# Performance work log

Measured on AMD Instinct MI355X. Metric: run time of the kernel, lower is better.

The kernel has to match this reference:

```python
import jax, jax.numpy as jnp
import numpy as np

N_NODES = 500_000
N_EDGES = 16_000_000


def setup_inputs() -> dict:
    key = jax.random.key(0)
    ks = jax.random.split(key, 10)
    x = jax.random.normal(ks[0], (N_NODES, 8), dtype=jnp.float32)
    edge_index = jax.random.randint(ks[1], (2, N_EDGES), 0, N_NODES, dtype=jnp.int64)
    W1_l = jax.random.normal(ks[2], (8, 32), dtype=jnp.float32) * 0.1
    W1_r = jax.random.normal(ks[3], (8, 32), dtype=jnp.float32) * 0.1
    b1 = jax.random.normal(ks[4], (32,), dtype=jnp.float32) * 0.1
    W2_l = jax.random.normal(ks[5], (32, 16), dtype=jnp.float32) * 0.1
    W2_r = jax.random.normal(ks[6], (32, 16), dtype=jnp.float32) * 0.1
    b2 = jax.random.normal(ks[7], (16,), dtype=jnp.float32) * 0.1
    W_out = jax.random.normal(ks[8], (16, 1), dtype=jnp.float32) * 0.1
    b_out = jax.random.normal(ks[9], (1,), dtype=jnp.float32) * 0.1
    return {"x": x, "edge_index": edge_index, "W1_l": W1_l, "W1_r": W1_r, "b1": b1,
            "W2_l": W2_l, "W2_r": W2_r, "b2": b2, "W_out": W_out, "b_out": b_out}


def _sage_conv(x, src, dst, deg_inv, W_l, W_r, b):
    # mean-aggregate neighbor features: gather x[src], scatter-add to dst, divide by degree
    agg = jax.ops.segment_sum(x[src], dst, num_segments=N_NODES)  # [N, d_in]
    mean_nb = agg * deg_inv[:, None]
    return mean_nb @ W_l + x @ W_r + b


def reference(x, edge_index, W1_l, W1_r, b1, W2_l, W2_r, b2, W_out, b_out):
    src, dst = edge_index[0], edge_index[1]
    # in-degree per target node (mean aggregation denominator), clamped at 1
    deg = jax.ops.segment_sum(jnp.ones((src.shape[0],), dtype=x.dtype), dst,
                              num_segments=N_NODES)
    deg_inv = 1.0 / jnp.maximum(deg, 1.0)
    h = jax.nn.relu(_sage_conv(x, src, dst, deg_inv, W1_l, W1_r, b1))
    # dropout(p=0.1) is identity at inference
    h = jax.nn.relu(_sage_conv(h, src, dst, deg_inv, W2_l, W2_r, b2))
    return jax.nn.sigmoid(h @ W_out + b_out)  # [N, 1]
```

## Files before the change

kernel.cpp:

```cpp
#include <hip/hip_runtime.h>
#include <hip/hip_fp16.h>
#include <math.h>

#define N_NODES 500000
#define N_EDGES 16000000

#define NCHUNK 256
#define CHUNK_E 62500
#define NBUCKET 2048
#define NPB 256
#define NB_USED 1954
#define BUCKET_CAP 9216

#define OFF_GH    0
#define OFF_TOT   2097152
#define OFF_BASE  2105344
#define OFF_ROW   2113600
#define OFF_DEG   4113600
#define OFF_XH8   6113600
#define OFF_PAIRS 10113664
#define OFF_H1P8  74113664
#define OFF_S2    82113664

typedef float v2f __attribute__((ext_vector_type(2)));

static __device__ inline float2 up2(unsigned int u) {
  __half2 h = *reinterpret_cast<__half2*>(&u);
  return __half22float2(h);
}
static __device__ inline unsigned int ph2(float a, float b) {
  __half2 h = __floats2half2_rn(a, b);
  return *reinterpret_cast<unsigned int*>(&h);
}
static __device__ inline unsigned int pk_fp8x4(float a, float b, float c, float d) {
  int u = __builtin_amdgcn_cvt_pk_fp8_f32(a, b, 0, false);
  u = __builtin_amdgcn_cvt_pk_fp8_f32(c, d, u, true);
  return (unsigned int)u;
}
static __device__ inline void acc8(float* a, uint2 g) {
  v2f f01 = __builtin_amdgcn_cvt_pk_f32_fp8((int)g.x, false);
  v2f f23 = __builtin_amdgcn_cvt_pk_f32_fp8((int)g.x, true);
  v2f f45 = __builtin_amdgcn_cvt_pk_f32_fp8((int)g.y, false);
  v2f f67 = __builtin_amdgcn_cvt_pk_f32_fp8((int)g.y, true);
  a[0] += f01.x; a[1] += f01.y; a[2] += f23.x; a[3] += f23.y;
  a[4] += f45.x; a[5] += f45.y; a[6] += f67.x; a[7] += f67.y;
}
static __device__ inline void acc16(float* a, uint4 g) {
  v2f f0 = __builtin_amdgcn_cvt_pk_f32_fp8((int)g.x, false);
  v2f f1 = __builtin_amdgcn_cvt_pk_f32_fp8((int)g.x, true);
  v2f f2 = __builtin_amdgcn_cvt_pk_f32_fp8((int)g.y, false);
  v2f f3 = __builtin_amdgcn_cvt_pk_f32_fp8((int)g.y, true);
  v2f f4 = __builtin_amdgcn_cvt_pk_f32_fp8((int)g.z, false);
  v2f f5 = __builtin_amdgcn_cvt_pk_f32_fp8((int)g.z, true);
  v2f f6 = __builtin_amdgcn_cvt_pk_f32_fp8((int)g.w, false);
  v2f f7 = __builtin_amdgcn_cvt_pk_f32_fp8((int)g.w, true);
  a[0] += f0.x;  a[1] += f0.y;  a[2] += f1.x;  a[3] += f1.y;
  a[4] += f2.x;  a[5] += f2.y;  a[6] += f3.x;  a[7] += f3.y;
  a[8] += f4.x;  a[9] += f4.y;  a[10] += f5.x; a[11] += f5.y;
  a[12] += f6.x; a[13] += f6.y; a[14] += f7.x; a[15] += f7.y;
}

__global__ __launch_bounds__(256) void k_xcast(const float* __restrict__ x,
                                               uint2* __restrict__ xh8) {
  int i = blockIdx.x * 256 + threadIdx.x;
  if (i >= N_NODES) return;
  const float4* xp = (const float4*)(x + (size_t)i * 8);
  float4 a = xp[0], b = xp[1];
  uint2 v;
  v.x = pk_fp8x4(a.x, a.y, a.z, a.w);
  v.y = pk_fp8x4(b.x, b.y, b.z, b.w);
  xh8[i] = v;
}

__global__ __launch_bounds__(256) void k_hist(const int* __restrict__ ei,
                                              int* __restrict__ gh) {
  __shared__ int hist[NBUCKET];
  int t = threadIdx.x;
  int c = blockIdx.x;
#pragma unroll
  for (int j = 0; j < NBUCKET / 256; j++) hist[t + j * 256] = 0;
  __syncthreads();
  int e0 = c * CHUNK_E;
  const int ngroups = CHUNK_E / 4;
  for (int g = t; g < ngroups; g += 256) {
    uint4 d4 = *(const uint4*)(ei + N_EDGES + e0 + g * 4);
    atomicAdd(&hist[d4.x >> 8], 1);
    atomicAdd(&hist[d4.y >> 8], 1);
    atomicAdd(&hist[d4.z >> 8], 1);
    atomicAdd(&hist[d4.w >> 8], 1);
  }
  __syncthreads();
#pragma unroll
  for (int j = 0; j < NBUCKET / 256; j++) {
    int b = t + j * 256;
    gh[c * NBUCKET + b] = hist[b];
  }
}

__global__ __launch_bounds__(256) void k_scanA(int* __restrict__ gh,
                                               int* __restrict__ tot) {
  int b = blockIdx.x * 256 + threadIdx.x;
  int run = 0;
  for (int c = 0; c < NCHUNK; c += 8) {
    int v[8];
#pragma unroll
    for (int j = 0; j < 8; j++) v[j] = gh[(c + j) * NBUCKET + b];
#pragma unroll
    for (int j = 0; j < 8; j++) {
      gh[(c + j) * NBUCKET + b] = run;
      run += v[j];
    }
  }
  tot[b] = run;
}

__global__ __launch_bounds__(256) void k_scanB(const int* __restrict__ tot,
                                               int* __restrict__ base) {
  __shared__ int lds[256];
  int t = threadIdx.x;
  int loc[8];
  int s = 0;
#pragma unroll
  for (int j = 0; j < 8; j++) {
    loc[j] = s;
    s += tot[t * 8 + j];
  }
  lds[t] = s;
  __syncthreads();
  for (int off = 1; off < 256; off <<= 1) {
    int v = (t >= off) ? lds[t - off] : 0;
    __syncthreads();
    lds[t] += v;
    __syncthreads();
  }
  int eb = (t > 0) ? lds[t - 1] : 0;
#pragma unroll
  for (int j = 0; j < 8; j++) base[t * 8 + j] = eb + loc[j];
  if (t == 255) base[NBUCKET] = lds[255];
}

__global__ __launch_bounds__(256) void k_scatter(const int* __restrict__ ei,
                                                 const int* __restrict__ gh,
                                                 const int* __restrict__ base,
                                                 unsigned int* __restrict__ pairs) {
  __shared__ int cur[NBUCKET];
  int t = threadIdx.x;
  int c = blockIdx.x;
#pragma unroll
  for (int j = 0; j < NBUCKET / 256; j++) {
    int b = t + j * 256;
    cur[b] = base[b] + gh[c * NBUCKET + b];
  }
  __syncthreads();
  int e0 = c * CHUNK_E;
  const int ngroups = CHUNK_E / 4;
  for (int g = t; g < ngroups; g += 256) {
    uint4 s4 = *(const uint4*)(ei + e0 + g * 4);
    uint4 d4 = *(const uint4*)(ei + N_EDGES + e0 + g * 4);
    unsigned int ss[4] = {s4.x, s4.y, s4.z, s4.w};
    unsigned int dd[4] = {d4.x, d4.y, d4.z, d4.w};
#pragma unroll
    for (int j = 0; j < 4; j++) {
      int b = dd[j] >> 8;
      int pos = atomicAdd(&cur[b], 1);
      pairs[pos] = ss[j] | ((dd[j] & 255u) << 19);
    }
  }
}

__global__ __launch_bounds__(256) void k_sort(unsigned int* __restrict__ pairs,
                                              const int* __restrict__ base,
                                              const int* __restrict__ tot,
                                              int* __restrict__ row,
                                              int* __restrict__ deg) {
  __shared__ unsigned int sp[BUCKET_CAP];
  __shared__ int hist[NPB];
  __shared__ int lds[NPB];
  __shared__ int cur[NPB];
  int t = threadIdx.x;
  int b = blockIdx.x;
  int e0 = base[b];
  int n = tot[b];
  if (n > BUCKET_CAP) n = BUCKET_CAP;
  for (int k = t; k < n; k += 256) sp[k] = pairs[e0 + k];
  hist[t] = 0;
  __syncthreads();
  for (int k = t; k < n; k += 256) atomicAdd(&hist[sp[k] >> 19], 1);
  __syncthreads();
  int h = hist[t];
  lds[t] = h;
  __syncthreads();
  for (int off = 1; off < 256; off <<= 1) {
    int v = (t >= off) ? lds[t - off] : 0;
    __syncthreads();
    lds[t] += v;
    __syncthreads();
  }
  int start = e0 + lds[t] - h;
  cur[t] = start;
  int i = (b << 8) + t;
  if (i < N_NODES) {
    row[i] = start;
    deg[i] = h;
  }
  __syncthreads();
  for (int k = t; k < n; k += 256) {
    unsigned int p = sp[k];
    int ld = (int)(p >> 19);
    int pos = atomicAdd(&cur[ld], 1);
    pairs[pos] = p & 0x7FFFFu;
  }
}

__global__ __launch_bounds__(256) void k_l1(
    const unsigned int* __restrict__ adj, const int* __restrict__ row,
    const int* __restrict__ deg, const uint2* __restrict__ xh8,
    const float* __restrict__ x,
    const float* __restrict__ W1l, const float* __restrict__ W1r,
    const float* __restrict__ b1,
    const float* __restrict__ W2l, const float* __restrict__ W2r,
    uint4* __restrict__ h1p8, unsigned int* __restrict__ s2) {
  __shared__ float sW1l[256], sW1r[256], sb1[32], sW2l[512], sW2r[512];
  int t = threadIdx.x;
  sW1l[t] = W1l[t];
  sW1r[t] = W1r[t];
  sW2l[t] = W2l[t];  sW2l[t + 256] = W2l[t + 256];
  sW2r[t] = W2r[t];  sW2r[t + 256] = W2r[t + 256];
  if (t < 32) sb1[t] = b1[t];
  __syncthreads();

  int i = blockIdx.x * 256 + t;
  if (i >= N_NODES) return;
  int rs = row[i];
  int d = deg[i];

  float acc[8] = {0, 0, 0, 0, 0, 0, 0, 0};
  int j = 0;
  for (; j + 4 <= d; j += 4) {
    int a0 = adj[rs + j + 0];
    int a1 = adj[rs + j + 1];
    int a2 = adj[rs + j + 2];
    int a3 = adj[rs + j + 3];
    uint2 g0 = xh8[a0], g1 = xh8[a1], g2 = xh8[a2], g3 = xh8[a3];
    acc8(acc, g0); acc8(acc, g1); acc8(acc, g2); acc8(acc, g3);
  }
  for (; j < d; j++) {
    uint2 g = xh8[adj[rs + j]];
    acc8(acc, g);
  }

  float dinv = 1.0f / fmaxf((float)d, 1.0f);
  float m[8];
#pragma unroll
  for (int f = 0; f < 8; f++) m[f] = acc[f] * dinv;
  const float4* xp = (const float4*)(x + (size_t)i * 8);
  float4 x0 = xp[0], x1 = xp[1];
  float xv[8] = {x0.x, x0.y, x0.z, x0.w, x1.x, x1.y, x1.z, x1.w};

  float h[32];
#pragma unroll
  for (int jj = 0; jj < 32; jj++) h[jj] = sb1[jj];
#pragma unroll
  for (int k = 0; k < 8; k++) {
#pragma unroll
    for (int jj = 0; jj < 32; jj++) {
      h[jj] = fmaf(m[k], sW1l[k * 32 + jj], h[jj]);
      h[jj] = fmaf(xv[k], sW1r[k * 32 + jj], h[jj]);
    }
  }
#pragma unroll
  for (int jj = 0; jj < 32; jj++) h[jj] = fmaxf(h[jj], 0.0f);

  float p[16], s[16];
#pragma unroll
  for (int jj = 0; jj < 16; jj++) { p[jj] = 0.0f; s[jj] = 0.0f; }
#pragma unroll
  for (int k = 0; k < 32; k++) {
#pragma unroll
    for (int jj = 0; jj < 16; jj++) {
      p[jj] = fmaf(h[k], sW2l[k * 16 + jj], p[jj]);
      s[jj] = fmaf(h[k], sW2r[k * 16 + jj], s[jj]);
    }
  }
  uint4 hv;
  hv.x = pk_fp8x4(p[0], p[1], p[2], p[3]);
  hv.y = pk_fp8x4(p[4], p[5], p[6], p[7]);
  hv.z = pk_fp8x4(p[8], p[9], p[10], p[11]);
  hv.w = pk_fp8x4(p[12], p[13], p[14], p[15]);
  h1p8[i] = hv;
  uint4* sp = (uint4*)(s2 + (size_t)i * 8);
  sp[0] = make_uint4(ph2(s[0], s[1]), ph2(s[2], s[3]), ph2(s[4], s[5]), ph2(s[6], s[7]));
  sp[1] = make_uint4(ph2(s[8], s[9]), ph2(s[10], s[11]), ph2(s[12], s[13]), ph2(s[14], s[15]));
}

__global__ __launch_bounds__(256) void k_l2(
    const unsigned int* __restrict__ adj, const int* __restrict__ row,
    const int* __restrict__ deg, const uint4* __restrict__ h1p8,
    const unsigned int* __restrict__ s2, const float* __restrict__ b2,
    const float* __restrict__ Wout, const float* __restrict__ bout,
    float* __restrict__ out) {
  __shared__ float sb2[16], sWo[16], sbo;
  int t = threadIdx.x;
  if (t < 16) { sb2[t] = b2[t]; sWo[t] = Wout[t]; }
  if (t == 0) sbo = bout[0];
  __syncthreads();

  int i = blockIdx.x * 256 + t;
  if (i >= N_NODES) return;
  int rs = row[i];
  int d = deg[i];

  float acc[16];
#pragma unroll
  for (int jj = 0; jj < 16; jj++) acc[jj] = 0.0f;
  int j = 0;
  for (; j + 4 <= d; j += 4) {
    int a0 = adj[rs + j + 0];
    int a1 = adj[rs + j + 1];
    int a2 = adj[rs + j + 2];
    int a3 = adj[rs + j + 3];
    uint4 g0 = h1p8[a0], g1 = h1p8[a1], g2 = h1p8[a2], g3 = h1p8[a3];
    acc16(acc, g0); acc16(acc, g1); acc16(acc, g2); acc16(acc, g3);
  }
  for (; j < d; j++) {
    uint4 g = h1p8[adj[rs + j]];
    acc16(acc, g);
  }

  float dinv = 1.0f / fmaxf((float)d, 1.0f);
  const uint4* sp = (const uint4*)(s2 + (size_t)i * 8);
  uint4 q0 = sp[0], q1 = sp[1];
  float2 s0 = up2(q0.x), s1 = up2(q0.y), s2v = up2(q0.z), s3 = up2(q0.w);
  float2 s4 = up2(q1.x), s5 = up2(q1.y), s6 = up2(q1.z), s7 = up2(q1.w);
  float sv[16] = {s0.x, s0.y, s1.x, s1.y, s2v.x, s2v.y, s3.x, s3.y,
                  s4.x, s4.y, s5.x, s5.y, s6.x, s6.y, s7.x, s7.y};
  float o = sbo;
#pragma unroll
  for (int c = 0; c < 16; c++) {
    float h2 = fmaxf(acc[c] * dinv + sv[c] + sb2[c], 0.0f);
    o = fmaf(h2, sWo[c], o);
  }
  out[i] = 1.0f / (1.0f + expf(-o));
}

extern "C" void kernel_launch(void* const* d_in, const int* in_sizes, int n_in,
                              void* d_out, int out_size, void* d_ws, size_t ws_size,
                              hipStream_t stream) {
  const float* x    = (const float*)d_in[0];
  const int*   ei   = (const int*)d_in[1];
  const float* W1l  = (const float*)d_in[2];
  const float* W1r  = (const float*)d_in[3];
  const float* b1   = (const float*)d_in[4];
  const float* W2l  = (const float*)d_in[5];
  const float* W2r  = (const float*)d_in[6];
  const float* b2   = (const float*)d_in[7];
  const float* Wout = (const float*)d_in[8];
  const float* bout = (const float*)d_in[9];
  float* out = (float*)d_out;

  char* ws = (char*)d_ws;
  int* gh    = (int*)(ws + OFF_GH);
  int* tot   = (int*)(ws + OFF_TOT);
  int* base  = (int*)(ws + OFF_BASE);
  int* row   = (int*)(ws + OFF_ROW);
  int* deg   = (int*)(ws + OFF_DEG);
  uint2* xh8 = (uint2*)(ws + OFF_XH8);
  unsigned int* pairs = (unsigned int*)(ws + OFF_PAIRS);
  uint4* h1p8 = (uint4*)(ws + OFF_H1P8);
  unsigned int* s2    = (unsigned int*)(ws + OFF_S2);

  k_xcast<<<NB_USED, 256, 0, stream>>>(x, xh8);
  k_hist<<<NCHUNK, 256, 0, stream>>>(ei, gh);
  k_scanA<<<8, 256, 0, stream>>>(gh, tot);
  k_scanB<<<1, 256, 0, stream>>>(tot, base);
  k_scatter<<<NCHUNK, 256, 0, stream>>>(ei, gh, base, pairs);
  k_sort<<<NBUCKET, 256, 0, stream>>>(pairs, base, tot, row, deg);
  k_l1<<<NB_USED, 256, 0, stream>>>(pairs, row, deg, xh8, x, W1l, W1r, b1,
                                    W2l, W2r, h1p8, s2);
  k_l2<<<NB_USED, 256, 0, stream>>>(pairs, row, deg, h1p8, s2, b2, Wout,
                                    bout, out);
}
```

Measured before the change: 1.033 ms.

## Replace single-pass bucket scatter with two-level radix partition in halves

```diff
diff --git a/kernel.cpp b/kernel.cpp
--- a/kernel.cpp
+++ b/kernel.cpp
@@ -5,22 +5,30 @@
 #define N_NODES 500000
 #define N_EDGES 16000000
 
-#define NCHUNK 256
-#define CHUNK_E 62500
 #define NBUCKET 2048
 #define NPB 256
+#define NSB 64
+#define NSLICE 32
 #define NB_USED 1954
 #define BUCKET_CAP 9216
 
-#define OFF_GH    0
-#define OFF_TOT   2097152
-#define OFF_BASE  2105344
-#define OFF_ROW   2113600
-#define OFF_DEG   4113600
-#define OFF_XH8   6113600
-#define OFF_PAIRS 10113664
-#define OFF_H1P8  74113664
-#define OFF_S2    82113664
+#define NCH_H 500
+#define CHUNK_H 32000
+#define NCH_A 1000
+#define CHUNK_A 16000
+
+#define OFF_TOT     0
+#define OFF_BASE    8192
+#define OFF_FCUR    16512
+#define OFF_SBCUR   24704
+#define OFF_AUXB    24960
+#define OFF_ROW     25600
+#define OFF_DEG     2025600
+#define OFF_XH8     4025600
+#define OFF_PAIRS   8025664
+#define OFF_AUX     72025664
+#define OFF_H1P8    72025664
+#define OFF_S2      80025664
 
 typedef float v2f __attribute__((ext_vector_type(2)));
 
@@ -73,16 +81,16 @@
 }
 
 __global__ __launch_bounds__(256) void k_hist(const int* __restrict__ ei,
-                                              int* __restrict__ gh) {
+                                              int* __restrict__ tot) {
   __shared__ int hist[NBUCKET];
   int t = threadIdx.x;
   int c = blockIdx.x;
 #pragma unroll
   for (int j = 0; j < NBUCKET / 256; j++) hist[t + j * 256] = 0;
   __syncthreads();
-  int e0 = c * CHUNK_E;
-  const int ngroups = CHUNK_E / 4;
-  for (int g = t; g < ngroups; g += 256) {
+  int e0 = c * CHUNK_H;
+  const int ng = CHUNK_H / 4;
+  for (int g = t; g < ng; g += 256) {
     uint4 d4 = *(const uint4*)(ei + N_EDGES + e0 + g * 4);
     atomicAdd(&hist[d4.x >> 8], 1);
     atomicAdd(&hist[d4.y >> 8], 1);
@@ -93,29 +101,15 @@
 #pragma unroll
   for (int j = 0; j < NBUCKET / 256; j++) {
     int b = t + j * 256;
-    gh[c * NBUCKET + b] = hist[b];
-  }
-}
-
-__global__ __launch_bounds__(256) void k_scanA(int* __restrict__ gh,
-                                               int* __restrict__ tot) {
-  int b = blockIdx.x * 256 + threadIdx.x;
-  int run = 0;
-  for (int c = 0; c < NCHUNK; c += 8) {
-    int v[8];
-#pragma unroll
-    for (int j = 0; j < 8; j++) v[j] = gh[(c + j) * NBUCKET + b];
-#pragma unroll
-    for (int j = 0; j < 8; j++) {
-      gh[(c + j) * NBUCKET + b] = run;
-      run += v[j];
-    }
-  }
-  tot[b] = run;
-}
-
-__global__ __launch_bounds__(256) void k_scanB(const int* __restrict__ tot,
-                                               int* __restrict__ base) {
+    if (hist[b]) atomicAdd(&tot[b], hist[b]);
+  }
+}
+
+__global__ __launch_bounds__(256) void k_scan(const int* __restrict__ tot,
+                                              int* __restrict__ base,
+                                              int* __restrict__ fineCur,
+                                              int* __restrict__ sbCur,
+                                              int* __restrict__ auxBase) {
   __shared__ int lds[256];
   int t = threadIdx.x;
   int loc[8];
@@ -135,42 +129,97 @@
   }
   int eb = (t > 0) ? lds[t - 1] : 0;
 #pragma unroll
-  for (int j = 0; j < 8; j++) base[t * 8 + j] = eb + loc[j];
+  for (int j = 0; j < 8; j++) {
+    int idx = t * 8 + j;
+    int v = eb + loc[j];
+    base[idx] = v;
+    fineCur[idx] = v;
+  }
   if (t == 255) base[NBUCKET] = lds[255];
-}
-
-__global__ __launch_bounds__(256) void k_scatter(const int* __restrict__ ei,
-                                                 const int* __restrict__ gh,
-                                                 const int* __restrict__ base,
-                                                 unsigned int* __restrict__ pairs) {
-  __shared__ int cur[NBUCKET];
+  if (t < NSB) {
+    int v = (t > 0) ? lds[t * 4 - 1] : 0;
+    if (t >= 32) v -= lds[127];
+    sbCur[t] = v;
+    auxBase[t] = v;
+  }
+}
+
+__global__ __launch_bounds__(256) void k_passA(const int* __restrict__ ei,
+                                               int* __restrict__ sbCur,
+                                               unsigned int* __restrict__ aux,
+                                               int half) {
+  __shared__ int hist[NSB];
+  __shared__ int cur[NSB];
   int t = threadIdx.x;
   int c = blockIdx.x;
-#pragma unroll
-  for (int j = 0; j < NBUCKET / 256; j++) {
-    int b = t + j * 256;
-    cur[b] = base[b] + gh[c * NBUCKET + b];
-  }
-  __syncthreads();
-  int e0 = c * CHUNK_E;
-  const int ngroups = CHUNK_E / 4;
-  for (int g = t; g < ngroups; g += 256) {
+  if (t < NSB) hist[t] = 0;
+  __syncthreads();
+  int e0 = c * CHUNK_A;
+  const int ng = CHUNK_A / 4;
+  for (int g = t; g < ng; g += 256) {
+    uint4 d4 = *(const uint4*)(ei + N_EDGES + e0 + g * 4);
+    unsigned int dd[4] = {d4.x, d4.y, d4.z, d4.w};
+#pragma unroll
+    for (int j = 0; j < 4; j++) {
+      int sb = (int)(dd[j] >> 13);
+      if ((sb >> 5) == half) atomicAdd(&hist[sb], 1);
+    }
+  }
+  __syncthreads();
+  if (t < NSB) cur[t] = atomicAdd(&sbCur[t], hist[t]);
+  __syncthreads();
+  for (int g = t; g < ng; g += 256) {
     uint4 s4 = *(const uint4*)(ei + e0 + g * 4);
     uint4 d4 = *(const uint4*)(ei + N_EDGES + e0 + g * 4);
     unsigned int ss[4] = {s4.x, s4.y, s4.z, s4.w};
     unsigned int dd[4] = {d4.x, d4.y, d4.z, d4.w};
 #pragma unroll
     for (int j = 0; j < 4; j++) {
-      int b = dd[j] >> 8;
-      int pos = atomicAdd(&cur[b], 1);
-      pairs[pos] = ss[j] | ((dd[j] & 255u) << 19);
+      int sb = (int)(dd[j] >> 13);
+      if ((sb >> 5) == half) {
+        int pos = atomicAdd(&cur[sb], 1);
+        aux[pos] = ss[j] | ((dd[j] & 8191u) << 19);
+      }
     }
+  }
+}
+
+__global__ __launch_bounds__(256) void k_passB(const unsigned int* __restrict__ aux,
+                                               const int* __restrict__ base,
+                                               const int* __restrict__ auxBase,
+                                               int* __restrict__ fineCur,
+                                               unsigned int* __restrict__ pairs,
+                                               int half) {
+  __shared__ int hist[32];
+  __shared__ int cur[32];
+  int t = threadIdx.x;
+  int sbl = blockIdx.x / NSLICE;
+  int sl = blockIdx.x % NSLICE;
+  int sb = half * 32 + sbl;
+  int aStart = auxBase[sb];
+  int len = base[(sb + 1) << 5] - base[sb << 5];
+  int per = (len + NSLICE - 1) / NSLICE;
+  int lo = sl * per;
+  int hi = lo + per;
+  if (hi > len) hi = len;
+  if (t < 32) hist[t] = 0;
+  __syncthreads();
+  for (int k = lo + t; k < hi; k += 256) {
+    unsigned int w = aux[aStart + k];
+    atomicAdd(&hist[w >> 27], 1);
+  }
+  __syncthreads();
+  if (t < 32) cur[t] = atomicAdd(&fineCur[(sb << 5) + t], hist[t]);
+  __syncthreads();
+  for (int k = lo + t; k < hi; k += 256) {
+    unsigned int w = aux[aStart + k];
+    int pos = atomicAdd(&cur[w >> 27], 1);
+    pairs[pos] = w;
   }
 }
 
 __global__ __launch_bounds__(256) void k_sort(unsigned int* __restrict__ pairs,
                                               const int* __restrict__ base,
-                                              const int* __restrict__ tot,
                                               int* __restrict__ row,
                                               int* __restrict__ deg) {
   __shared__ unsigned int sp[BUCKET_CAP];
@@ -180,12 +229,12 @@
   int t = threadIdx.x;
   int b = blockIdx.x;
   int e0 = base[b];
-  int n = tot[b];
+  int n = base[b + 1] - e0;
   if (n > BUCKET_CAP) n = BUCKET_CAP;
   for (int k = t; k < n; k += 256) sp[k] = pairs[e0 + k];
   hist[t] = 0;
   __syncthreads();
-  for (int k = t; k < n; k += 256) atomicAdd(&hist[sp[k] >> 19], 1);
+  for (int k = t; k < n; k += 256) atomicAdd(&hist[(sp[k] >> 19) & 255u], 1);
   __syncthreads();
   int h = hist[t];
   lds[t] = h;
@@ -206,7 +255,7 @@
   __syncthreads();
   for (int k = t; k < n; k += 256) {
     unsigned int p = sp[k];
-    int ld = (int)(p >> 19);
+    int ld = (int)((p >> 19) & 255u);
     int pos = atomicAdd(&cur[ld], 1);
     pairs[pos] = p & 0x7FFFFu;
   }
@@ -359,22 +408,29 @@
   float* out = (float*)d_out;
 
   char* ws = (char*)d_ws;
-  int* gh    = (int*)(ws + OFF_GH);
-  int* tot   = (int*)(ws + OFF_TOT);
-  int* base  = (int*)(ws + OFF_BASE);
-  int* row   = (int*)(ws + OFF_ROW);
-  int* deg   = (int*)(ws + OFF_DEG);
-  uint2* xh8 = (uint2*)(ws + OFF_XH8);
+  int* tot     = (int*)(ws + OFF_TOT);
+  int* base    = (int*)(ws + OFF_BASE);
+  int* fineCur = (int*)(ws + OFF_FCUR);
+  int* sbCur   = (int*)(ws + OFF_SBCUR);
+  int* auxBase = (int*)(ws + OFF_AUXB);
+  int* row     = (int*)(ws + OFF_ROW);
+  int* deg     = (int*)(ws + OFF_DEG);
+  uint2* xh8   = (uint2*)(ws + OFF_XH8);
   unsigned int* pairs = (unsigned int*)(ws + OFF_PAIRS);
-  uint4* h1p8 = (uint4*)(ws + OFF_H1P8);
-  unsigned int* s2    = (unsigned int*)(ws + OFF_S2);
+  unsigned int* aux   = (unsigned int*)(ws + OFF_AUX);
+  uint4* h1p8  = (uint4*)(ws + OFF_H1P8);
+  unsigned int* s2 = (unsigned int*)(ws + OFF_S2);
+
+  hipMemsetAsync(tot, 0, NBUCKET * sizeof(int), stream);
 
   k_xcast<<<NB_USED, 256, 0, stream>>>(x, xh8);
-  k_hist<<<NCHUNK, 256, 0, stream>>>(ei, gh);
-  k_scanA<<<8, 256, 0, stream>>>(gh, tot);
-  k_scanB<<<1, 256, 0, stream>>>(tot, base);
-  k_scatter<<<NCHUNK, 256, 0, stream>>>(ei, gh, base, pairs);
-  k_sort<<<NBUCKET, 256, 0, stream>>>(pairs, base, tot, row, deg);
+  k_hist<<<NCH_H, 256, 0, stream>>>(ei, tot);
+  k_scan<<<1, 256, 0, stream>>>(tot, base, fineCur, sbCur, auxBase);
+  k_passA<<<NCH_A, 256, 0, stream>>>(ei, sbCur, aux, 0);
+  k_passB<<<32 * NSLICE, 256, 0, stream>>>(aux, base, auxBase, fineCur, pairs, 0);
+  k_passA<<<NCH_A, 256, 0, stream>>>(ei, sbCur, aux, 1);
+  k_passB<<<32 * NSLICE, 256, 0, stream>>>(aux, base, auxBase, fineCur, pairs, 1);
+  k_sort<<<NBUCKET, 256, 0, stream>>>(pairs, base, row, deg);
   k_l1<<<NB_USED, 256, 0, stream>>>(pairs, row, deg, xh8, x, W1l, W1r, b1,
                                     W2l, W2r, h1p8, s2);
   k_l2<<<NB_USED, 256, 0, stream>>>(pairs, row, deg, h1p8, s2, b2, Wout,
```

Measured after the change: 898.4 us. -13.0%, faster.
